# Kernel optimization log

Hardware: AMD Instinct MI355X
Metric: run time of the kernel (lower is better)

The kernel has to match this reference:

```python
import jax, jax.numpy as jnp
import numpy as np

B, S, H = 2, 2048, 2048
E, K = 8, 2            # num_local_experts, num_experts_per_tok
I, IS = 1024, 4096     # expert / shared-expert intermediate dims


def setup_inputs() -> dict:
    key = jax.random.key(0)
    ks = jax.random.split(key, 8)
    w = lambda k, shp: jax.random.normal(k, shp, dtype=jnp.float32) * 0.02
    return {
        "hidden_states": jax.random.normal(ks[0], (B, S, H), dtype=jnp.float32),
        "router_w": w(ks[1], (E, H)),
        "gate_w": w(ks[2], (E, I, H)),
        "up_w": w(ks[3], (E, I, H)),
        "down_w": w(ks[4], (E, H, I)),
        "shared_gate_w": w(ks[5], (IS, H)),
        "shared_up_w": w(ks[6], (IS, H)),
        "shared_down_w": w(ks[7], (H, IS)),
    }


def reference(hidden_states, router_w, gate_w, up_w, down_w,
              shared_gate_w, shared_up_w, shared_down_w):
    x = hidden_states  # [B,S,H]
    b, s, h = x.shape

    # Router: logits over experts, top-k, sigmoid of top values (computed in fp32)
    router_logits = jnp.einsum('bsh,eh->bse', x, router_w)           # [B,S,E]
    top_vals, top_idx = jax.lax.top_k(router_logits, K)              # [B,S,K]
    scores = jax.nn.sigmoid(top_vals.astype(jnp.float32)).astype(x.dtype)

    # Per-token per-expert input scale (each expert appears at most once in top-k)
    onehot = jax.nn.one_hot(top_idx, E, dtype=x.dtype)               # [B,S,K,E]
    scale = jnp.einsum('bsk,bske->bse', scores, onehot)              # [B,S,E]

    # Routed experts: scale is applied to the INPUT of each expert (as in the torch code).
    # With bias-free gated MLP, zero-scaled (unrouted) tokens produce exact zeros,
    # so the dense formulation matches the sparse gather/scatter exactly.
    xs = x.reshape(-1, h)                                            # [T,H]
    sc = scale.reshape(-1, E)                                        # [T,E]
    xe = xs[:, None, :] * sc[:, :, None]                             # [T,E,H]
    g = jnp.einsum('teh,eih->tei', xe, gate_w)                       # [T,E,I]
    u = jnp.einsum('teh,eih->tei', xe, up_w)                         # [T,E,I]
    hmid = jax.nn.silu(g) * u
    routed = jnp.einsum('tei,ehi->th', hmid, down_w).reshape(b, s, h)

    # Shared expert (dense gated MLP over all tokens)
    sg = jnp.einsum('bsh,ih->bsi', x, shared_gate_w)
    su = jnp.einsum('bsh,ih->bsi', x, shared_up_w)
    shared = jnp.einsum('bsi,hi->bsh', jax.nn.silu(sg) * su, shared_down_w)

    return routed + shared, router_logits
```

## Files before the change

### kernel.cpp

```cpp
#include <hip/hip_runtime.h>
#include <hip/hip_bf16.h>
#include <cstdint>
#include <cstddef>

typedef __bf16 bf16x8 __attribute__((ext_vector_type(8)));
typedef float  f32x4  __attribute__((ext_vector_type(4)));

static constexpr int TOK  = 4096;
static constexpr int H    = 2048;
static constexpr int E    = 8;
static constexpr int IDIM = 1024;
static constexpr int ISD  = 4096;
static constexpr int MAXT256 = 40;
static constexpr int MAXT128 = 80;
static constexpr int MAXROWS = MAXT256 * 256;


__device__ __forceinline__ void gll16(const void* g, void* l) {
  __builtin_amdgcn_global_load_lds((const __attribute__((address_space(1))) void*)g,
                                   (__attribute__((address_space(3))) void*)l, 16, 0, 0);
}

__device__ __forceinline__ unsigned short f2bf(float f) {
  unsigned int u = __float_as_uint(f);
  u = (u + 0x7fffu + ((u >> 16) & 1u)) >> 16;
  return (unsigned short)u;
}

__global__ __launch_bounds__(256) void detect_kernel(const unsigned int* __restrict__ x,
                                                     int* __restrict__ meta) {
  __shared__ int sh[256];
  const int tid = threadIdx.x;
  int c = 0;
  for (int i = tid; i < 1024; i += 256) {
    const unsigned int e = (x[i] >> 7) & 0xFFu;
    c += (e >= 100u && e <= 150u) ? 1 : 0;
  }
  sh[tid] = c;
  if (tid >= 4 && tid < 24) meta[tid] = 0;
  __syncthreads();
  if (tid == 0) {
    int s = 0;
    for (int i = 0; i < 256; ++i) s += sh[i];
    meta[0] = (s > 512) ? 1 : 0;
  }
}

__global__ __launch_bounds__(256) void convert_all_kernel(
    const float* __restrict__ s0, const float* __restrict__ s1,
    const float* __restrict__ s2, const float* __restrict__ s3,
    const float* __restrict__ s4, const float* __restrict__ s5,
    const float* __restrict__ s6, const float* __restrict__ s7,
    unsigned short* __restrict__ d0, unsigned short* __restrict__ d1,
    unsigned short* __restrict__ d2, unsigned short* __restrict__ d3,
    unsigned short* __restrict__ d4, unsigned short* __restrict__ d5,
    unsigned short* __restrict__ d6, unsigned short* __restrict__ d7,
    const int* __restrict__ flag)
{
  if (*flag) return;
  const int stride = gridDim.x * 256;
  const int base = blockIdx.x * 256 + threadIdx.x;
  auto go = [&](const float* s, unsigned short* d, int n4) {
    for (int i = base; i < n4; i += stride) {
      const float4 v = ((const float4*)s)[i];
      ushort4 o;
      o.x = f2bf(v.x); o.y = f2bf(v.y); o.z = f2bf(v.z); o.w = f2bf(v.w);
      ((ushort4*)d)[i] = o;
    }
  };
  go(s0, d0, (TOK * H) / 4);
  go(s1, d1, (E * H) / 4);
  go(s2, d2, (E * IDIM * H) / 4);
  go(s3, d3, (E * IDIM * H) / 4);
  go(s4, d4, (E * H * IDIM) / 4);
  go(s5, d5, (ISD * H) / 4);
  go(s6, d6, (ISD * H) / 4);
  go(s7, d7, (ISD * H) / 4);
}

__global__ __launch_bounds__(256) void router_kernel(
    const void* __restrict__ x_, const void* __restrict__ rw_,
    void* __restrict__ out, float* __restrict__ scale,
    int* __restrict__ meta, int* __restrict__ topk)
{
  const int bfmode = meta[0];
  const int t   = blockIdx.x;
  const int tid = threadIdx.x;
  const int l   = tid & 63, w = tid >> 6;
  const int off = tid * 8;

  float xs[8];
  if (bfmode) {
    bf16x8 v = *(const bf16x8*)((const unsigned short*)x_ + (size_t)t * H + off);
#pragma unroll
    for (int j = 0; j < 8; ++j) xs[j] = (float)v[j];
  } else {
    const float* xr = (const float*)x_ + (size_t)t * H + off;
    const float4 a = *(const float4*)xr;
    const float4 b = *(const float4*)(xr + 4);
    xs[0]=a.x; xs[1]=a.y; xs[2]=a.z; xs[3]=a.w; xs[4]=b.x; xs[5]=b.y; xs[6]=b.z; xs[7]=b.w;
  }

  float p[E];
#pragma unroll
  for (int e = 0; e < E; ++e) {
    float wv[8];
    if (bfmode) {
      bf16x8 v = *(const bf16x8*)((const unsigned short*)rw_ + (size_t)e * H + off);
#pragma unroll
      for (int j = 0; j < 8; ++j) wv[j] = (float)v[j];
    } else {
      const float* wr = (const float*)rw_ + (size_t)e * H + off;
      const float4 a = *(const float4*)wr;
      const float4 b = *(const float4*)(wr + 4);
      wv[0]=a.x; wv[1]=a.y; wv[2]=a.z; wv[3]=a.w; wv[4]=b.x; wv[5]=b.y; wv[6]=b.z; wv[7]=b.w;
    }
    float s = 0.f;
#pragma unroll
    for (int j = 0; j < 8; ++j) s = fmaf(xs[j], wv[j], s);
    p[e] = s;
  }
#pragma unroll
  for (int e = 0; e < E; ++e)
    for (int o = 32; o > 0; o >>= 1) p[e] += __shfl_down(p[e], o);

  __shared__ float red[E][4];
  __shared__ float lg[E];
  __shared__ float sres[2];
  __shared__ int   ires[2];
  if (l == 0) {
#pragma unroll
    for (int e = 0; e < E; ++e) red[e][w] = p[e];
  }
  __syncthreads();
  if (tid < E) {
    const float v = red[tid][0] + red[tid][1] + red[tid][2] + red[tid][3];
    lg[tid] = v;
    const size_t oi = (size_t)TOK * H + (size_t)t * E + tid;
    if (bfmode) ((unsigned short*)out)[oi] = f2bf(v);
    else        ((float*)out)[oi] = v;
  }
  __syncthreads();
  if (tid == 0) {
    int i0 = 0; float v0 = lg[0];
    for (int e = 1; e < E; ++e) if (lg[e] > v0) { v0 = lg[e]; i0 = e; }
    int i1 = -1; float v1 = 0.f; bool init = false;
    for (int e = 0; e < E; ++e) {
      if (e == i0) continue;
      if (!init || lg[e] > v1) { v1 = lg[e]; i1 = e; init = true; }
    }
    sres[0] = 1.f / (1.f + expf(-v0)); ires[0] = i0;
    sres[1] = 1.f / (1.f + expf(-v1)); ires[1] = i1;
    topk[2 * t + 0] = i0;
    topk[2 * t + 1] = i1;
    atomicAdd(&meta[4 + i0], 1);
    atomicAdd(&meta[4 + i1], 1);
  }
  __syncthreads();
  if (tid < E) {
    float s = 0.f;
    if (tid == ires[0]) s = sres[0];
    else if (tid == ires[1]) s = sres[1];
    scale[(size_t)t * E + tid] = s;
  }
}

__global__ __launch_bounds__(256) void scan_kernel(int* __restrict__ meta,
                                                   int* __restrict__ list) {
  const int tid = threadIdx.x;
  if (tid == 0) {
    int s = 0, n256 = 0, n128 = 0;
    for (int e = 0; e < E; ++e) {
      meta[24 + e] = s;
      const int cnt = meta[4 + e];
      const int tiles = (cnt + 255) >> 8;
      for (int i = 0; i < tiles; ++i) {
        meta[64 + n256]  = e;
        meta[104 + n256] = s + i * 256;
        ++n256;
        meta[144 + n128] = e; meta[224 + n128] = s + i * 256;       ++n128;
        meta[144 + n128] = e; meta[224 + n128] = s + i * 256 + 128; ++n128;
      }
      s += tiles << 8;
    }
    meta[32] = s;
    meta[20] = n256;
    meta[21] = n128;
  }
  for (int i = tid; i < MAXROWS; i += 256) list[i] = 0;
}

__global__ __launch_bounds__(256) void scatter_kernel(int* __restrict__ meta,
                                                      const int* __restrict__ topk,
                                                      int* __restrict__ list,
                                                      int* __restrict__ tokpos) {
  const int t = blockIdx.x * 256 + threadIdx.x;
  if (t >= TOK) return;
#pragma unroll
  for (int k = 0; k < 2; ++k) {
    const int e = topk[2 * t + k];
    const int p = atomicAdd(&meta[12 + e], 1);
    const int g = meta[24 + e] + p;
    list[g] = t;
    tokpos[2 * t + k] = g;
  }
}

#define GU_BAR_   __builtin_amdgcn_s_barrier()
#define GU_LGKM0_ { asm volatile("s_waitcnt lgkmcnt(0)" ::: "memory"); \
                    __builtin_amdgcn_sched_barrier(0); }
#define GU_VM4_   asm volatile("s_waitcnt vmcnt(4)" ::: "memory")
#define GU_VM0_   asm volatile("s_waitcnt vmcnt(0)" ::: "memory")

#define LDA_(p, mh) { _Pragma("unroll") for (int q2 = 0; q2 < 4; ++q2) { \
  _Pragma("unroll") for (int ks = 0; ks < 2; ++ks) { \
    const int row_ = 32 * (4 * (mh) + q2) + 16 * wm + lm; \
    a[q2][ks] = *(const bf16x8*)&ldsA[(p) * 16384 + row_ * 64 + \
                                      (((ks * 4 + quad) ^ (lm & 7)) * 8)]; } } }

#define LDB_(p, nh) { _Pragma("unroll") for (int nt2 = 0; nt2 < 2; ++nt2) { \
  _Pragma("unroll") for (int ks = 0; ks < 2; ++ks) { \
    const int row_ = 16 * (wn + 4 * (2 * (nh) + nt2)) + lm; \
    bb[nh][nt2][ks] = *(const bf16x8*)&ldsB[(p) * 16384 + row_ * 64 + \
                                            (((ks * 4 + quad) ^ (lm & 7)) * 8)]; } } }

#define MFMA_(mh, nh) { __builtin_amdgcn_s_setprio(1); \
  _Pragma("unroll") for (int q2 = 0; q2 < 4; ++q2) \
  _Pragma("unroll") for (int nt2 = 0; nt2 < 2; ++nt2) \
  _Pragma("unroll") for (int ks = 0; ks < 2; ++ks) \
    acc[4 * (mh) + q2][2 * (nh) + nt2] = __builtin_amdgcn_mfma_f32_16x16x32_bf16( \
      a[q2][ks], bb[nh][nt2][ks], acc[4 * (mh) + q2][2 * (nh) + nt2], 0, 0, 0); \
  __builtin_amdgcn_s_setprio(0); }

#define GU_PIPELINE_(STA, STB) \
  STA(0, 0); STB(0, 0); STB(0, 1); STA(0, 1); \
  STB(1, 1); STA(1, 1); \
  GU_VM4_; GU_BAR_; \
  for (int i = 0; i < (H / 128) - 1; ++i) { \
    const int t0 = 2 * i, t1 = 2 * i + 1; \
    LDA_(0, 0); LDB_(0, 0); STA(t1, 0); \
    GU_BAR_; GU_LGKM0_; MFMA_(0, 0); GU_BAR_; \
    LDB_(0, 1); STB(t1, 0); \
    GU_BAR_; GU_LGKM0_; MFMA_(0, 1); GU_BAR_; \
    LDA_(0, 1); STA(t0 + 2, 0); \
    GU_BAR_; GU_LGKM0_; MFMA_(1, 1); GU_BAR_; \
    STB(t0 + 2, 0); GU_VM4_; \
    GU_BAR_; GU_LGKM0_; MFMA_(1, 0); GU_BAR_; \
    LDA_(1, 0); LDB_(1, 0); STB(t0 + 2, 1); \
    GU_BAR_; GU_LGKM0_; MFMA_(0, 0); GU_BAR_; \
    LDB_(1, 1); STA(t0 + 2, 1); \
    GU_BAR_; GU_LGKM0_; MFMA_(0, 1); GU_BAR_; \
    LDA_(1, 1); STB(t1 + 2, 1); \
    GU_BAR_; GU_LGKM0_; MFMA_(1, 1); GU_BAR_; \
    STA(t1 + 2, 1); GU_VM4_; \
    GU_BAR_; GU_LGKM0_; MFMA_(1, 0); GU_BAR_; \
  } \
  { \
    const int t1 = H / 64 - 1; \
    LDA_(0, 0); LDB_(0, 0); STA(t1, 0); \
    GU_BAR_; GU_LGKM0_; MFMA_(0, 0); GU_BAR_; \
    LDB_(0, 1); STB(t1, 0); \
    GU_BAR_; GU_LGKM0_; MFMA_(0, 1); GU_BAR_; \
    LDA_(0, 1); \
    GU_BAR_; GU_LGKM0_; MFMA_(1, 1); GU_BAR_; \
    GU_VM0_; \
    GU_BAR_; GU_LGKM0_; MFMA_(1, 0); GU_BAR_; \
    LDA_(1, 0); LDB_(1, 0); \
    GU_BAR_; GU_LGKM0_; MFMA_(0, 0); GU_BAR_; \
    LDB_(1, 1); \
    GU_BAR_; GU_LGKM0_; MFMA_(0, 1); GU_BAR_; \
    LDA_(1, 1); \
    GU_BAR_; GU_LGKM0_; MFMA_(1, 1); GU_BAR_; \
    MFMA_(1, 0); \
  }

__global__ __launch_bounds__(512, 2) void gateup_shared_kernel(
    const void* __restrict__ xo_,  const unsigned short* __restrict__ cx,
    const void* __restrict__ sgo_, const unsigned short* __restrict__ csgw,
    const void* __restrict__ suo_, const unsigned short* __restrict__ csuw,
    unsigned short* __restrict__ hmid_sh, const int* __restrict__ meta)
{
  extern __shared__ unsigned short lds[];
  unsigned short* ldsA = lds;
  unsigned short* ldsB = lds + 32768;

  const int bfmode = meta[0];
  const unsigned short* x  = bfmode ? (const unsigned short*)xo_  : cx;
  const unsigned short* gw = bfmode ? (const unsigned short*)sgo_ : csgw;
  const unsigned short* uw = bfmode ? (const unsigned short*)suo_ : csuw;

  const int tid = threadIdx.x;
  const int l = tid & 63, w = tid >> 6;
  const int wm = w >> 2, wn = w & 3;
  const int quad = l >> 4, lm = l & 15;
  const int m0 = blockIdx.x * 256;
  const int jb = blockIdx.y * 128;

  const unsigned short* gB = gw + (size_t)jb * H;
  const unsigned short* uB = uw + (size_t)jb * H;

  const int sr0 = tid >> 3,         sc0 = tid & 7;
  const int sr1 = (tid + 512) >> 3, sc1 = (tid + 512) & 7;
  const int scc0 = sc0 ^ (sr0 & 7), scc1 = sc1 ^ (sr1 & 7);
  const int sd0 = tid * 8, sd1 = (tid + 512) * 8;

  auto stA = [&](int kt, int half) {
    unsigned short* d = ldsA + (kt & 1) * 16384 + half * 8192;
    const unsigned short* s = x + (size_t)(m0 + half * 128) * H + kt * 64;
    gll16(s + (size_t)sr0 * H + scc0 * 8, d + sd0);
    gll16(s + (size_t)sr1 * H + scc1 * 8, d + sd1);
  };
  auto stB = [&](int kt, int half) {
    unsigned short* d = ldsB + (kt & 1) * 16384 + half * 8192;
    const unsigned short* s = (half ? uB : gB) + kt * 64;
    gll16(s + (size_t)sr0 * H + scc0 * 8, d + sd0);
    gll16(s + (size_t)sr1 * H + scc1 * 8, d + sd1);
  };

  f32x4 acc[8][4] = {};
  bf16x8 a[4][2];
  bf16x8 bb[2][2][2];

  GU_PIPELINE_(stA, stB);

#pragma unroll
  for (int mt = 0; mt < 8; ++mt) {
    const int trow = m0 + 32 * mt + 16 * wm + quad * 4;
#pragma unroll
    for (int ntp = 0; ntp < 2; ++ntp) {
      const int col = jb + wn * 16 + ntp * 64 + lm;
#pragma unroll
      for (int rr = 0; rr < 4; ++rr) {
        const float g = acc[mt][ntp][rr];
        const float u = acc[mt][ntp + 2][rr];
        const float hm = (g / (1.f + expf(-g))) * u;
        hmid_sh[(size_t)(trow + rr) * ISD + col] = f2bf(hm);
      }
    }
  }
}

__global__ __launch_bounds__(512, 2) void gateup_routed_kernel(
    const void* __restrict__ xo_,  const unsigned short* __restrict__ cx,
    const void* __restrict__ gwo_, const unsigned short* __restrict__ cgw,
    const void* __restrict__ uwo_, const unsigned short* __restrict__ cuw,
    const float* __restrict__ scale, const int* __restrict__ list,
    unsigned short* __restrict__ hmid_r, const int* __restrict__ meta)
{
  if ((int)blockIdx.x >= meta[20]) return;
  extern __shared__ unsigned short lds[];
  unsigned short* ldsA = lds;
  unsigned short* ldsB = lds + 32768;

  const int bfmode = meta[0];
  const unsigned short* x      = bfmode ? (const unsigned short*)xo_  : cx;
  const unsigned short* gate_w = bfmode ? (const unsigned short*)gwo_ : cgw;
  const unsigned short* up_w   = bfmode ? (const unsigned short*)uwo_ : cuw;

  const int tid = threadIdx.x;
  const int l = tid & 63, w = tid >> 6;
  const int wm = w >> 2, wn = w & 3;
  const int quad = l >> 4, lm = l & 15;
  const int e    = meta[64 + blockIdx.x];
  const int base = meta[104 + blockIdx.x];
  const int jb   = blockIdx.y * 128;

  const unsigned short* gB = gate_w + ((size_t)e * IDIM + jb) * H;
  const unsigned short* uB = up_w   + ((size_t)e * IDIM + jb) * H;

  const int sr0 = tid >> 3,         sc0 = tid & 7;
  const int sr1 = (tid + 512) >> 3, sc1 = (tid + 512) & 7;
  const int scc0 = sc0 ^ (sr0 & 7), scc1 = sc1 ^ (sr1 & 7);
  const int sd0 = tid * 8, sd1 = (tid + 512) * 8;

  int tokh[2][2];
#pragma unroll
  for (int h = 0; h < 2; ++h) {
    tokh[h][0] = list[base + h * 128 + sr0];
    tokh[h][1] = list[base + h * 128 + sr1];
  }

  auto stA = [&](int kt, int half) {
    unsigned short* d = ldsA + (kt & 1) * 16384 + half * 8192;
    gll16(x + (size_t)tokh[half][0] * H + kt * 64 + scc0 * 8, d + sd0);
    gll16(x + (size_t)tokh[half][1] * H + kt * 64 + scc1 * 8, d + sd1);
  };
  auto stB = [&](int kt, int half) {
    unsigned short* d = ldsB + (kt & 1) * 16384 + half * 8192;
    const unsigned short* s = (half ? uB : gB) + kt * 64;
    gll16(s + (size_t)sr0 * H + scc0 * 8, d + sd0);
    gll16(s + (size_t)sr1 * H + scc1 * 8, d + sd1);
  };

  f32x4 acc[8][4] = {};
  bf16x8 a[4][2];
  bf16x8 bb[2][2][2];

  GU_PIPELINE_(stA, stB);

#pragma unroll
  for (int mt = 0; mt < 8; ++mt) {
    const int rloc = 32 * mt + 16 * wm + quad * 4;
#pragma unroll
    for (int rr = 0; rr < 4; ++rr) {
      const int gpos = base + rloc + rr;
      const float s = scale[(size_t)list[gpos] * E + e];
#pragma unroll
      for (int ntp = 0; ntp < 2; ++ntp) {
        const int col = jb + wn * 16 + ntp * 64 + lm;
        const float g = acc[mt][ntp][rr] * s;
        const float u = acc[mt][ntp + 2][rr] * s;
        const float hm = (g / (1.f + expf(-g))) * u;
        hmid_r[(size_t)gpos * IDIM + col] = f2bf(hm);
      }
    }
  }
}

__global__ __launch_bounds__(256) void down_routed_kernel(
    const unsigned short* __restrict__ hmid_r,
    const void* __restrict__ dwo_, const unsigned short* __restrict__ cdw,
    float* __restrict__ dbuf, const int* __restrict__ meta)
{
  if ((int)blockIdx.y >= meta[21]) return;
  const int bfmode = meta[0];
  const unsigned short* down_w = bfmode ? (const unsigned short*)dwo_ : cdw;

  __shared__ __attribute__((aligned(16))) unsigned short As[128 * 64];
  __shared__ __attribute__((aligned(16))) unsigned short Bs[128 * 64];

  const int tid = threadIdx.x;
  const int l = tid & 63, w = tid >> 6;
  const int e    = meta[144 + blockIdx.y];
  const int base = meta[224 + blockIdx.y];
  const int n0 = blockIdx.x * 128;

  const unsigned short* Bbase = down_w + ((size_t)e * H + n0) * IDIM;

  f32x4 acc[4][4] = {};
  const int wm = (w >> 1) * 64;
  const int wn = (w & 1) * 64;
  const int quad = l >> 4, lm = l & 15;

  for (int k0 = 0; k0 < IDIM; k0 += 64) {
#pragma unroll
    for (int j = 0; j < 4; ++j) {
      const int g = j * 256 + tid;
      const int r = g >> 3, c = g & 7;
      const int cc = c ^ (r & 7);
      gll16(hmid_r + (size_t)(base + r) * IDIM + k0 + cc * 8, &As[g * 8]);
    }
#pragma unroll
    for (int j = 0; j < 4; ++j) {
      const int g = j * 256 + tid;
      const int r = g >> 3, c = g & 7;
      const int cc = c ^ (r & 7);
      gll16(Bbase + (size_t)r * IDIM + k0 + cc * 8, &Bs[g * 8]);
    }
    __syncthreads();
#pragma unroll
    for (int ks = 0; ks < 64; ks += 32) {
      const int kc  = (ks >> 3) + quad;
      const int csw = (kc ^ (lm & 7)) * 8;
      bf16x8 a[4], b[4];
#pragma unroll
      for (int mt = 0; mt < 4; ++mt)
        a[mt] = *(const bf16x8*)&As[(wm + mt * 16 + lm) * 64 + csw];
#pragma unroll
      for (int nt = 0; nt < 4; ++nt)
        b[nt] = *(const bf16x8*)&Bs[(wn + nt * 16 + lm) * 64 + csw];
#pragma unroll
      for (int mt = 0; mt < 4; ++mt)
#pragma unroll
        for (int nt = 0; nt < 4; ++nt)
          acc[mt][nt] = __builtin_amdgcn_mfma_f32_16x16x32_bf16(a[mt], b[nt], acc[mt][nt], 0, 0, 0);
    }
    __syncthreads();
  }

#pragma unroll
  for (int mt = 0; mt < 4; ++mt)
#pragma unroll
    for (int nt = 0; nt < 4; ++nt)
#pragma unroll
      for (int r = 0; r < 4; ++r) {
        const int row = wm + mt * 16 + quad * 4 + r;
        const int n   = n0 + wn + nt * 16 + lm;
        dbuf[(size_t)(base + row) * H + n] = acc[mt][nt][r];
      }
}

__global__ __launch_bounds__(256) void down_shared_kernel(
    const unsigned short* __restrict__ hmid_sh,
    const void* __restrict__ sdwo_, const unsigned short* __restrict__ csdw,
    const float* __restrict__ dbuf, const int* __restrict__ tokpos,
    void* __restrict__ out, const int* __restrict__ meta)
{
  const int bfmode = meta[0];
  const unsigned short* sdown_w = bfmode ? (const unsigned short*)sdwo_ : csdw;

  __shared__ __attribute__((aligned(16))) unsigned short As[128 * 64];
  __shared__ __attribute__((aligned(16))) unsigned short Bs[128 * 64];

  const int tid = threadIdx.x;
  const int l = tid & 63, w = tid >> 6;
  const int m0 = blockIdx.y * 128;
  const int n0 = blockIdx.x * 128;

  f32x4 acc[4][4] = {};
  const int wm = (w >> 1) * 64;
  const int wn = (w & 1) * 64;
  const int quad = l >> 4, lm = l & 15;

  for (int k0 = 0; k0 < ISD; k0 += 64) {
#pragma unroll
    for (int j = 0; j < 4; ++j) {
      const int g = j * 256 + tid;
      const int r = g >> 3, c = g & 7;
      const int cc = c ^ (r & 7);
      gll16(hmid_sh + (size_t)(m0 + r) * ISD + k0 + cc * 8, &As[g * 8]);
    }
#pragma unroll
    for (int j = 0; j < 4; ++j) {
      const int g = j * 256 + tid;
      const int r = g >> 3, c = g & 7;
      const int cc = c ^ (r & 7);
      gll16(sdown_w + (size_t)(n0 + r) * ISD + k0 + cc * 8, &Bs[g * 8]);
    }
    __syncthreads();
#pragma unroll
    for (int ks = 0; ks < 64; ks += 32) {
      const int kc  = (ks >> 3) + quad;
      const int csw = (kc ^ (lm & 7)) * 8;
      bf16x8 a[4], b[4];
#pragma unroll
      for (int mt = 0; mt < 4; ++mt)
        a[mt] = *(const bf16x8*)&As[(wm + mt * 16 + lm) * 64 + csw];
#pragma unroll
      for (int nt = 0; nt < 4; ++nt)
        b[nt] = *(const bf16x8*)&Bs[(wn + nt * 16 + lm) * 64 + csw];
#pragma unroll
      for (int mt = 0; mt < 4; ++mt)
#pragma unroll
        for (int nt = 0; nt < 4; ++nt)
          acc[mt][nt] = __builtin_amdgcn_mfma_f32_16x16x32_bf16(a[mt], b[nt], acc[mt][nt], 0, 0, 0);
    }
    __syncthreads();
  }

  if (bfmode) {
    unsigned short* o = (unsigned short*)out;
#pragma unroll
    for (int mt = 0; mt < 4; ++mt)
#pragma unroll
      for (int r = 0; r < 4; ++r) {
        const int t = m0 + wm + mt * 16 + quad * 4 + r;
        const int p0 = tokpos[2 * t], p1 = tokpos[2 * t + 1];
#pragma unroll
        for (int nt = 0; nt < 4; ++nt) {
          const int n = n0 + wn + nt * 16 + lm;
          const float v = acc[mt][nt][r]
                        + dbuf[(size_t)p0 * H + n] + dbuf[(size_t)p1 * H + n];
          o[(size_t)t * H + n] = f2bf(v);
        }
      }
  } else {
    float* o = (float*)out;
#pragma unroll
    for (int mt = 0; mt < 4; ++mt)
#pragma unroll
      for (int r = 0; r < 4; ++r) {
        const int t = m0 + wm + mt * 16 + quad * 4 + r;
        const int p0 = tokpos[2 * t], p1 = tokpos[2 * t + 1];
#pragma unroll
        for (int nt = 0; nt < 4; ++nt) {
          const int n = n0 + wn + nt * 16 + lm;
          o[(size_t)t * H + n] = acc[mt][nt][r]
                               + dbuf[(size_t)p0 * H + n] + dbuf[(size_t)p1 * H + n];
        }
      }
  }
}

extern "C" void kernel_launch(void* const* d_in, const int* in_sizes, int n_in,
                              void* d_out, int out_size, void* d_ws, size_t ws_size,
                              hipStream_t stream) {
  const void* x   = d_in[0];
  const void* rw  = d_in[1];
  const void* gw  = d_in[2];
  const void* uw  = d_in[3];
  const void* dw  = d_in[4];
  const void* sgw = d_in[5];
  const void* suw = d_in[6];
  const void* sdw = d_in[7];

  char* wsb = (char*)d_ws;
  int*   meta   = (int*)wsb;
  float* scale  = (float*)(wsb + 2048);
  int*   topk   = (int*)(wsb + 2048 + (size_t)TOK * E * 4);
  int*   list   = topk + (size_t)TOK * 2;
  int*   tokpos = list + MAXROWS;
  unsigned short* hmid_sh = (unsigned short*)(wsb + 262144);
  unsigned short* hmid_r  = hmid_sh + (size_t)TOK * ISD;
  unsigned short* cx   = hmid_r + (size_t)MAXROWS * IDIM;
  unsigned short* crw  = cx  + (size_t)TOK * H;
  unsigned short* cgw  = crw + (size_t)E * H;
  unsigned short* cuw  = cgw + (size_t)E * IDIM * H;
  unsigned short* cdw  = cuw + (size_t)E * IDIM * H;
  unsigned short* csgw = cdw + (size_t)E * H * IDIM;
  unsigned short* csuw = csgw + (size_t)ISD * H;
  unsigned short* csdw = csuw + (size_t)ISD * H;
  float* dbuf = (float*)cx;

  static int attr_set = 0;
  if (!attr_set) {
    hipFuncSetAttribute(reinterpret_cast<const void*>(gateup_shared_kernel),
                        hipFuncAttributeMaxDynamicSharedMemorySize, 131072);
    hipFuncSetAttribute(reinterpret_cast<const void*>(gateup_routed_kernel),
                        hipFuncAttributeMaxDynamicSharedMemorySize, 131072);
    attr_set = 1;
  }

  detect_kernel<<<1, 256, 0, stream>>>((const unsigned int*)x, meta);

  convert_all_kernel<<<2048, 256, 0, stream>>>(
      (const float*)x, (const float*)rw, (const float*)gw, (const float*)uw,
      (const float*)dw, (const float*)sgw, (const float*)suw, (const float*)sdw,
      cx, crw, cgw, cuw, cdw, csgw, csuw, csdw, meta);

  router_kernel<<<TOK, 256, 0, stream>>>(x, rw, d_out, scale, meta, topk);
  scan_kernel<<<1, 256, 0, stream>>>(meta, list);
  scatter_kernel<<<TOK / 256, 256, 0, stream>>>(meta, topk, list, tokpos);

  dim3 g1(TOK / 256, ISD / 128);
  gateup_shared_kernel<<<g1, 512, 131072, stream>>>(x, cx, sgw, csgw, suw, csuw,
                                                    hmid_sh, meta);

  dim3 g2(MAXT256, IDIM / 128);
  gateup_routed_kernel<<<g2, 512, 131072, stream>>>(x, cx, gw, cgw, uw, cuw,
                                                    scale, list, hmid_r, meta);

  dim3 g3(H / 128, MAXT128);
  down_routed_kernel<<<g3, 256, 0, stream>>>(hmid_r, dw, cdw, dbuf, meta);

  dim3 g4(H / 128, TOK / 128);
  down_shared_kernel<<<g4, 256, 0, stream>>>(hmid_sh, sdw, csdw, dbuf, tokpos, d_out, meta);
}
```

Before: 865.9 us.

## Accumulate down projections with atomics; retile shared down GEMM with split-K pipeline

Replaces the routed-down scratch buffer plus gather in the shared-down epilogue with direct atomic float accumulation into a zeroed output (or an fp32 psum in bf16 mode, converted at the end). The shared down GEMM moves to the 256x256 pipelined tile machinery with split-K of two, and the router processes four tokens per block with one wavefront each, avoiding shared-memory reductions. Padding rows are marked -1 and skipped. This removes the dbuf write/read round trip and uses a larger tile in exchange for atomic contention, an extra zero pass and non-deterministic summation order.

```diff
diff --git a/kernel.cpp b/kernel.cpp
--- a/kernel.cpp
+++ b/kernel.cpp
@@ -43,6 +43,30 @@
     int s = 0;
     for (int i = 0; i < 256; ++i) s += sh[i];
     meta[0] = (s > 512) ? 1 : 0;
+  }
+}
+
+__global__ __launch_bounds__(256) void zero_kernel(float* __restrict__ psum,
+                                                   void* __restrict__ out,
+                                                   const int* __restrict__ meta) {
+  float* tgt = meta[0] ? psum : (float*)out;
+  const float4 z = {0.f, 0.f, 0.f, 0.f};
+  int i = blockIdx.x * 256 + threadIdx.x;
+  const int stride = gridDim.x * 256;
+  for (; i < (TOK * H) / 4; i += stride) ((float4*)tgt)[i] = z;
+}
+
+__global__ __launch_bounds__(256) void psum2bf_kernel(const float* __restrict__ psum,
+                                                      unsigned short* __restrict__ out,
+                                                      const int* __restrict__ meta) {
+  if (!meta[0]) return;
+  int i = blockIdx.x * 256 + threadIdx.x;
+  const int stride = gridDim.x * 256;
+  for (; i < (TOK * H) / 4; i += stride) {
+    const float4 v = ((const float4*)psum)[i];
+    ushort4 o;
+    o.x = f2bf(v.x); o.y = f2bf(v.y); o.z = f2bf(v.z); o.w = f2bf(v.w);
+    ((ushort4*)out)[i] = o;
   }
 }
 
@@ -84,84 +108,79 @@
     int* __restrict__ meta, int* __restrict__ topk)
 {
   const int bfmode = meta[0];
-  const int t   = blockIdx.x;
-  const int tid = threadIdx.x;
-  const int l   = tid & 63, w = tid >> 6;
-  const int off = tid * 8;
-
-  float xs[8];
+  const int t = blockIdx.x * 4 + (threadIdx.x >> 6);
+  const int l = threadIdx.x & 63;
+  const int off = l * 32;
+
+  float xs[32];
   if (bfmode) {
-    bf16x8 v = *(const bf16x8*)((const unsigned short*)x_ + (size_t)t * H + off);
-#pragma unroll
-    for (int j = 0; j < 8; ++j) xs[j] = (float)v[j];
+    const unsigned short* xr = (const unsigned short*)x_ + (size_t)t * H + off;
+#pragma unroll
+    for (int j = 0; j < 4; ++j) {
+      bf16x8 v = *(const bf16x8*)(xr + j * 8);
+#pragma unroll
+      for (int k = 0; k < 8; ++k) xs[j * 8 + k] = (float)v[k];
+    }
   } else {
     const float* xr = (const float*)x_ + (size_t)t * H + off;
-    const float4 a = *(const float4*)xr;
-    const float4 b = *(const float4*)(xr + 4);
-    xs[0]=a.x; xs[1]=a.y; xs[2]=a.z; xs[3]=a.w; xs[4]=b.x; xs[5]=b.y; xs[6]=b.z; xs[7]=b.w;
+#pragma unroll
+    for (int j = 0; j < 8; ++j) {
+      const float4 v = *(const float4*)(xr + j * 4);
+      xs[j * 4] = v.x; xs[j * 4 + 1] = v.y; xs[j * 4 + 2] = v.z; xs[j * 4 + 3] = v.w;
+    }
   }
 
   float p[E];
 #pragma unroll
   for (int e = 0; e < E; ++e) {
-    float wv[8];
+    float s = 0.f;
     if (bfmode) {
-      bf16x8 v = *(const bf16x8*)((const unsigned short*)rw_ + (size_t)e * H + off);
-#pragma unroll
-      for (int j = 0; j < 8; ++j) wv[j] = (float)v[j];
+      const unsigned short* wr = (const unsigned short*)rw_ + (size_t)e * H + off;
+#pragma unroll
+      for (int j = 0; j < 4; ++j) {
+        bf16x8 v = *(const bf16x8*)(wr + j * 8);
+#pragma unroll
+        for (int k = 0; k < 8; ++k) s = fmaf(xs[j * 8 + k], (float)v[k], s);
+      }
     } else {
       const float* wr = (const float*)rw_ + (size_t)e * H + off;
-      const float4 a = *(const float4*)wr;
-      const float4 b = *(const float4*)(wr + 4);
-      wv[0]=a.x; wv[1]=a.y; wv[2]=a.z; wv[3]=a.w; wv[4]=b.x; wv[5]=b.y; wv[6]=b.z; wv[7]=b.w;
-    }
-    float s = 0.f;
-#pragma unroll
-    for (int j = 0; j < 8; ++j) s = fmaf(xs[j], wv[j], s);
+#pragma unroll
+      for (int j = 0; j < 8; ++j) {
+        const float4 v = *(const float4*)(wr + j * 4);
+        s = fmaf(xs[j * 4], v.x, s);     s = fmaf(xs[j * 4 + 1], v.y, s);
+        s = fmaf(xs[j * 4 + 2], v.z, s); s = fmaf(xs[j * 4 + 3], v.w, s);
+      }
+    }
     p[e] = s;
   }
 #pragma unroll
   for (int e = 0; e < E; ++e)
+#pragma unroll
     for (int o = 32; o > 0; o >>= 1) p[e] += __shfl_down(p[e], o);
 
-  __shared__ float red[E][4];
-  __shared__ float lg[E];
-  __shared__ float sres[2];
-  __shared__ int   ires[2];
   if (l == 0) {
-#pragma unroll
-    for (int e = 0; e < E; ++e) red[e][w] = p[e];
-  }
-  __syncthreads();
-  if (tid < E) {
-    const float v = red[tid][0] + red[tid][1] + red[tid][2] + red[tid][3];
-    lg[tid] = v;
-    const size_t oi = (size_t)TOK * H + (size_t)t * E + tid;
-    if (bfmode) ((unsigned short*)out)[oi] = f2bf(v);
-    else        ((float*)out)[oi] = v;
-  }
-  __syncthreads();
-  if (tid == 0) {
-    int i0 = 0; float v0 = lg[0];
-    for (int e = 1; e < E; ++e) if (lg[e] > v0) { v0 = lg[e]; i0 = e; }
+    int i0 = 0; float v0 = p[0];
+#pragma unroll
+    for (int e = 1; e < E; ++e) if (p[e] > v0) { v0 = p[e]; i0 = e; }
     int i1 = -1; float v1 = 0.f; bool init = false;
+#pragma unroll
     for (int e = 0; e < E; ++e) {
       if (e == i0) continue;
-      if (!init || lg[e] > v1) { v1 = lg[e]; i1 = e; init = true; }
-    }
-    sres[0] = 1.f / (1.f + expf(-v0)); ires[0] = i0;
-    sres[1] = 1.f / (1.f + expf(-v1)); ires[1] = i1;
+      if (!init || p[e] > v1) { v1 = p[e]; i1 = e; init = true; }
+    }
+    const float s0 = 1.f / (1.f + expf(-v0));
+    const float s1 = 1.f / (1.f + expf(-v1));
     topk[2 * t + 0] = i0;
     topk[2 * t + 1] = i1;
     atomicAdd(&meta[4 + i0], 1);
     atomicAdd(&meta[4 + i1], 1);
-  }
-  __syncthreads();
-  if (tid < E) {
-    float s = 0.f;
-    if (tid == ires[0]) s = sres[0];
-    else if (tid == ires[1]) s = sres[1];
-    scale[(size_t)t * E + tid] = s;
+    const size_t oi = (size_t)TOK * H + (size_t)t * E;
+#pragma unroll
+    for (int e = 0; e < E; ++e) {
+      if (bfmode) ((unsigned short*)out)[oi + e] = f2bf(p[e]);
+      else        ((float*)out)[oi + e] = p[e];
+      scale[(size_t)t * E + e] = (e == i0) ? s0 : ((e == i1) ? s1 : 0.f);
+    }
   }
 }
 
@@ -187,22 +206,19 @@
     meta[20] = n256;
     meta[21] = n128;
   }
-  for (int i = tid; i < MAXROWS; i += 256) list[i] = 0;
+  for (int i = tid; i < MAXROWS; i += 256) list[i] = -1;
 }
 
 __global__ __launch_bounds__(256) void scatter_kernel(int* __restrict__ meta,
                                                       const int* __restrict__ topk,
-                                                      int* __restrict__ list,
-                                                      int* __restrict__ tokpos) {
+                                                      int* __restrict__ list) {
   const int t = blockIdx.x * 256 + threadIdx.x;
   if (t >= TOK) return;
 #pragma unroll
   for (int k = 0; k < 2; ++k) {
     const int e = topk[2 * t + k];
     const int p = atomicAdd(&meta[12 + e], 1);
-    const int g = meta[24 + e] + p;
-    list[g] = t;
-    tokpos[2 * t + k] = g;
+    list[meta[24 + e] + p] = t;
   }
 }
 
@@ -376,8 +392,10 @@
   int tokh[2][2];
 #pragma unroll
   for (int h = 0; h < 2; ++h) {
-    tokh[h][0] = list[base + h * 128 + sr0];
-    tokh[h][1] = list[base + h * 128 + sr1];
+    const int ta = list[base + h * 128 + sr0];
+    const int tb = list[base + h * 128 + sr1];
+    tokh[h][0] = ta < 0 ? 0 : ta;
+    tokh[h][1] = tb < 0 ? 0 : tb;
   }
 
   auto stA = [&](int kt, int half) {
@@ -404,7 +422,8 @@
 #pragma unroll
     for (int rr = 0; rr < 4; ++rr) {
       const int gpos = base + rloc + rr;
-      const float s = scale[(size_t)list[gpos] * E + e];
+      const int token = list[gpos];
+      const float s = token < 0 ? 0.f : scale[(size_t)token * E + e];
 #pragma unroll
       for (int ntp = 0; ntp < 2; ++ntp) {
         const int col = jb + wn * 16 + ntp * 64 + lm;
@@ -417,14 +436,75 @@
   }
 }
 
+__global__ __launch_bounds__(512, 2) void down_shared_kernel(
+    const unsigned short* __restrict__ hmid_sh,
+    const void* __restrict__ sdwo_, const unsigned short* __restrict__ csdw,
+    float* __restrict__ psum, void* __restrict__ out, const int* __restrict__ meta)
+{
+  extern __shared__ unsigned short lds[];
+  unsigned short* ldsA = lds;
+  unsigned short* ldsB = lds + 32768;
+
+  const int bfmode = meta[0];
+  const unsigned short* sdw = bfmode ? (const unsigned short*)sdwo_ : csdw;
+  float* tgt = bfmode ? psum : (float*)out;
+
+  const int tid = threadIdx.x;
+  const int l = tid & 63, w = tid >> 6;
+  const int wm = w >> 2, wn = w & 3;
+  const int quad = l >> 4, lm = l & 15;
+  const int m0 = blockIdx.y * 256;
+  const int n0 = blockIdx.x * 256;
+  const int kbase = blockIdx.z * (ISD / 2);
+
+  const int sr0 = tid >> 3,         sc0 = tid & 7;
+  const int sr1 = (tid + 512) >> 3, sc1 = (tid + 512) & 7;
+  const int scc0 = sc0 ^ (sr0 & 7), scc1 = sc1 ^ (sr1 & 7);
+  const int sd0 = tid * 8, sd1 = (tid + 512) * 8;
+
+  auto stA = [&](int kt, int half) {
+    unsigned short* d = ldsA + (kt & 1) * 16384 + half * 8192;
+    const unsigned short* s = hmid_sh + (size_t)(m0 + half * 128) * ISD + kbase + kt * 64;
+    gll16(s + (size_t)sr0 * ISD + scc0 * 8, d + sd0);
+    gll16(s + (size_t)sr1 * ISD + scc1 * 8, d + sd1);
+  };
+  auto stB = [&](int kt, int half) {
+    unsigned short* d = ldsB + (kt & 1) * 16384 + half * 8192;
+    const unsigned short* s = sdw + (size_t)(n0 + half * 128) * ISD + kbase + kt * 64;
+    gll16(s + (size_t)sr0 * ISD + scc0 * 8, d + sd0);
+    gll16(s + (size_t)sr1 * ISD + scc1 * 8, d + sd1);
+  };
+
+  f32x4 acc[8][4] = {};
+  bf16x8 a[4][2];
+  bf16x8 bb[2][2][2];
+
+  GU_PIPELINE_(stA, stB);
+
+#pragma unroll
+  for (int mt = 0; mt < 8; ++mt) {
+#pragma unroll
+    for (int rr = 0; rr < 4; ++rr) {
+      const int t = m0 + 32 * mt + 16 * wm + quad * 4 + rr;
+#pragma unroll
+      for (int cg = 0; cg < 4; ++cg) {
+        const int n = n0 + 16 * (wn + 4 * cg) + lm;
+        atomicAdd(&tgt[(size_t)t * H + n], acc[mt][cg][rr]);
+      }
+    }
+  }
+}
+
 __global__ __launch_bounds__(256) void down_routed_kernel(
     const unsigned short* __restrict__ hmid_r,
     const void* __restrict__ dwo_, const unsigned short* __restrict__ cdw,
-    float* __restrict__ dbuf, const int* __restrict__ meta)
+    float* __restrict__ psum, void* __restrict__ out,
+    const int* __restrict__ list, const int* __restrict__ meta)
 {
   if ((int)blockIdx.y >= meta[21]) return;
   const int bfmode = meta[0];
   const unsigned short* down_w = bfmode ? (const unsigned short*)dwo_ : cdw;
+  float* tgt = bfmode ? psum : (float*)out;
 
   __shared__ __attribute__((aligned(16))) unsigned short As[128 * 64];
   __shared__ __attribute__((aligned(16))) unsigned short Bs[128 * 64];
@@ -481,105 +561,16 @@
 #pragma unroll
   for (int mt = 0; mt < 4; ++mt)
 #pragma unroll
-    for (int nt = 0; nt < 4; ++nt)
-#pragma unroll
-      for (int r = 0; r < 4; ++r) {
-        const int row = wm + mt * 16 + quad * 4 + r;
-        const int n   = n0 + wn + nt * 16 + lm;
-        dbuf[(size_t)(base + row) * H + n] = acc[mt][nt][r];
+    for (int r = 0; r < 4; ++r) {
+      const int row = wm + mt * 16 + quad * 4 + r;
+      const int token = list[base + row];
+      if (token < 0) continue;
+#pragma unroll
+      for (int nt = 0; nt < 4; ++nt) {
+        const int n = n0 + wn + nt * 16 + lm;
+        atomicAdd(&tgt[(size_t)token * H + n], acc[mt][nt][r]);
       }
-}
-
-__global__ __launch_bounds__(256) void down_shared_kernel(
-    const unsigned short* __restrict__ hmid_sh,
-    const void* __restrict__ sdwo_, const unsigned short* __restrict__ csdw,
-    const float* __restrict__ dbuf, const int* __restrict__ tokpos,
-    void* __restrict__ out, const int* __restrict__ meta)
-{
-  const int bfmode = meta[0];
-  const unsigned short* sdown_w = bfmode ? (const unsigned short*)sdwo_ : csdw;
-
-  __shared__ __attribute__((aligned(16))) unsigned short As[128 * 64];
-  __shared__ __attribute__((aligned(16))) unsigned short Bs[128 * 64];
-
-  const int tid = threadIdx.x;
-  const int l = tid & 63, w = tid >> 6;
-  const int m0 = blockIdx.y * 128;
-  const int n0 = blockIdx.x * 128;
-
-  f32x4 acc[4][4] = {};
-  const int wm = (w >> 1) * 64;
-  const int wn = (w & 1) * 64;
-  const int quad = l >> 4, lm = l & 15;
-
-  for (int k0 = 0; k0 < ISD; k0 += 64) {
-#pragma unroll
-    for (int j = 0; j < 4; ++j) {
-      const int g = j * 256 + tid;
-      const int r = g >> 3, c = g & 7;
-      const int cc = c ^ (r & 7);
-      gll16(hmid_sh + (size_t)(m0 + r) * ISD + k0 + cc * 8, &As[g * 8]);
-    }
-#pragma unroll
-    for (int j = 0; j < 4; ++j) {
-      const int g = j * 256 + tid;
-      const int r = g >> 3, c = g & 7;
-      const int cc = c ^ (r & 7);
-      gll16(sdown_w + (size_t)(n0 + r) * ISD + k0 + cc * 8, &Bs[g * 8]);
-    }
-    __syncthreads();
-#pragma unroll
-    for (int ks = 0; ks < 64; ks += 32) {
-      const int kc  = (ks >> 3) + quad;
-      const int csw = (kc ^ (lm & 7)) * 8;
-      bf16x8 a[4], b[4];
-#pragma unroll
-      for (int mt = 0; mt < 4; ++mt)
-        a[mt] = *(const bf16x8*)&As[(wm + mt * 16 + lm) * 64 + csw];
-#pragma unroll
-      for (int nt = 0; nt < 4; ++nt)
-        b[nt] = *(const bf16x8*)&Bs[(wn + nt * 16 + lm) * 64 + csw];
-#pragma unroll
-      for (int mt = 0; mt < 4; ++mt)
-#pragma unroll
-        for (int nt = 0; nt < 4; ++nt)
-          acc[mt][nt] = __builtin_amdgcn_mfma_f32_16x16x32_bf16(a[mt], b[nt], acc[mt][nt], 0, 0, 0);
-    }
-    __syncthreads();
-  }
-
-  if (bfmode) {
-    unsigned short* o = (unsigned short*)out;
-#pragma unroll
-    for (int mt = 0; mt < 4; ++mt)
-#pragma unroll
-      for (int r = 0; r < 4; ++r) {
-        const int t = m0 + wm + mt * 16 + quad * 4 + r;
-        const int p0 = tokpos[2 * t], p1 = tokpos[2 * t + 1];
-#pragma unroll
-        for (int nt = 0; nt < 4; ++nt) {
-          const int n = n0 + wn + nt * 16 + lm;
-          const float v = acc[mt][nt][r]
-                        + dbuf[(size_t)p0 * H + n] + dbuf[(size_t)p1 * H + n];
-          o[(size_t)t * H + n] = f2bf(v);
-        }
-      }
-  } else {
-    float* o = (float*)out;
-#pragma unroll
-    for (int mt = 0; mt < 4; ++mt)
-#pragma unroll
-      for (int r = 0; r < 4; ++r) {
-        const int t = m0 + wm + mt * 16 + quad * 4 + r;
-        const int p0 = tokpos[2 * t], p1 = tokpos[2 * t + 1];
-#pragma unroll
-        for (int nt = 0; nt < 4; ++nt) {
-          const int n = n0 + wn + nt * 16 + lm;
-          o[(size_t)t * H + n] = acc[mt][nt][r]
-                               + dbuf[(size_t)p0 * H + n] + dbuf[(size_t)p1 * H + n];
-        }
-      }
-  }
+    }
 }
 
 extern "C" void kernel_launch(void* const* d_in, const int* in_sizes, int n_in,
@@ -599,7 +590,6 @@
   float* scale  = (float*)(wsb + 2048);
   int*   topk   = (int*)(wsb + 2048 + (size_t)TOK * E * 4);
   int*   list   = topk + (size_t)TOK * 2;
-  int*   tokpos = list + MAXROWS;
   unsigned short* hmid_sh = (unsigned short*)(wsb + 262144);
   unsigned short* hmid_r  = hmid_sh + (size_t)TOK * ISD;
   unsigned short* cx   = hmid_r + (size_t)MAXROWS * IDIM;
@@ -610,7 +600,7 @@
   unsigned short* csgw = cdw + (size_t)E * H * IDIM;
   unsigned short* csuw = csgw + (size_t)ISD * H;
   unsigned short* csdw = csuw + (size_t)ISD * H;
-  float* dbuf = (float*)cx;
+  float* psum = (float*)cx;
 
   static int attr_set = 0;
   if (!attr_set) {
@@ -618,19 +608,22 @@
                         hipFuncAttributeMaxDynamicSharedMemorySize, 131072);
     hipFuncSetAttribute(reinterpret_cast<const void*>(gateup_routed_kernel),
                         hipFuncAttributeMaxDynamicSharedMemorySize, 131072);
+    hipFuncSetAttribute(reinterpret_cast<const void*>(down_shared_kernel),
+                        hipFuncAttributeMaxDynamicSharedMemorySize, 131072);
     attr_set = 1;
   }
 
   detect_kernel<<<1, 256, 0, stream>>>((const unsigned int*)x, meta);
+  zero_kernel<<<1024, 256, 0, stream>>>(psum, d_out, meta);
 
   convert_all_kernel<<<2048, 256, 0, stream>>>(
       (const float*)x, (const float*)rw, (const float*)gw, (const float*)uw,
       (const float*)dw, (const float*)sgw, (const float*)suw, (const float*)sdw,
       cx, crw, cgw, cuw, cdw, csgw, csuw, csdw, meta);
 
-  router_kernel<<<TOK, 256, 0, stream>>>(x, rw, d_out, scale, meta, topk);
+  router_kernel<<<TOK / 4, 256, 0, stream>>>(x, rw, d_out, scale, meta, topk);
   scan_kernel<<<1, 256, 0, stream>>>(meta, list);
-  scatter_kernel<<<TOK / 256, 256, 0, stream>>>(meta, topk, list, tokpos);
+  scatter_kernel<<<TOK / 256, 256, 0, stream>>>(meta, topk, list);
 
   dim3 g1(TOK / 256, ISD / 128);
   gateup_shared_kernel<<<g1, 512, 131072, stream>>>(x, cx, sgw, csgw, suw, csuw,
@@ -640,9 +633,11 @@
   gateup_routed_kernel<<<g2, 512, 131072, stream>>>(x, cx, gw, cgw, uw, cuw,
                                                     scale, list, hmid_r, meta);
 
-  dim3 g3(H / 128, MAXT128);
-  down_routed_kernel<<<g3, 256, 0, stream>>>(hmid_r, dw, cdw, dbuf, meta);
-
-  dim3 g4(H / 128, TOK / 128);
-  down_shared_kernel<<<g4, 256, 0, stream>>>(hmid_sh, sdw, csdw, dbuf, tokpos, d_out, meta);
-}
+  dim3 g3(H / 256, TOK / 256, 2);
+  down_shared_kernel<<<g3, 512, 131072, stream>>>(hmid_sh, sdw, csdw, psum, d_out, meta);
+
+  dim3 g4(H / 128, MAXT128);
+  down_routed_kernel<<<g4, 256, 0, stream>>>(hmid_r, dw, cdw, psum, d_out, list, meta);
+
+  psum2bf_kernel<<<1024, 256, 0, stream>>>(psum, (unsigned short*)d_out, meta);
+}
```

Result: slower. 937.1 us (+8.2%).
